# Kernel tuning notes

Measured on AMD Instinct MI355X. Metric: run time of the kernel, lower is better.

Reference implementation:

```python
import jax, jax.numpy as jnp
import numpy as np

EPS = 1e-5
H = 8  # num_heads

def ln(x, g, b):
    m = x.mean(-1, keepdims=True)
    v = ((x - m) ** 2).mean(-1, keepdims=True)
    return (x - m) / jnp.sqrt(v + EPS) * g + b

def gca(qf, kf, p):
    # Gated cross-modal attention (eval mode, dropout off, mask all-True => no mask)
    (nqg, nqb, nkg, nkb, wq, bq, wk, bk, wv, bv, wo, bo,
     wgp, bgp, g1w, g1b, glng, glnb, g2w, g2b) = p
    B, Sq, _ = qf.shape
    Sk = kf.shape[1]
    E = wq.shape[1]
    D = E // H
    qn = ln(qf, nqg, nqb)
    kn = ln(kf, nkg, nkb)
    q = (qn @ wq + bq).reshape(B, Sq, H, D)
    k = (kn @ wk + bk).reshape(B, Sk, H, D)
    v = (kn @ wv + bv).reshape(B, Sk, H, D)
    scores = jnp.einsum('bqhd,bkhd->bhqk', q, k) * (D ** -0.5)
    w = jax.nn.softmax(scores, axis=-1)          # [B,H,Sq,Sk]
    ctx = jnp.einsum('bhqk,bkhd->bqhd', w, v).reshape(B, Sq, E)
    att = ctx @ wo + bo                          # cross-attention output
    qp = qf @ wgp + bgp                          # query projected for gating
    h = jnp.concatenate([qp, att], axis=-1) @ g1w + g1b
    gate = jax.nn.sigmoid(jax.nn.gelu(ln(h, glng, glnb), approximate=False) @ g2w + g2b)
    return qp + gate * att, w

def ff(x, lng, lnb, w1, b1, w2, b2):
    y = jax.nn.gelu(ln(x, lng, lnb) @ w1 + b1, approximate=False)
    return x + (y @ w2 + b2)

def setup_inputs() -> dict:
    B, Sv, St, Vd, Td, F = 8, 1024, 512, 1024, 768, 512
    keys = iter(jax.random.split(jax.random.key(0), 80))
    def nrm(shape):
        return jax.random.normal(next(keys), shape, jnp.float32) * 0.02
    d = {}
    d['vision_features'] = jax.random.normal(next(keys), (B, Sv, Vd), jnp.float32)
    d['text_features'] = jax.random.normal(next(keys), (B, St, Td), jnp.float32)
    def attn_params(pfx, qd, kd, e):
        d[pfx + 'nq_g'] = jnp.ones(qd); d[pfx + 'nq_b'] = jnp.zeros(qd)
        d[pfx + 'nk_g'] = jnp.ones(kd); d[pfx + 'nk_b'] = jnp.zeros(kd)
        d[pfx + 'wq'] = nrm((qd, e)); d[pfx + 'bq'] = jnp.zeros(e)
        d[pfx + 'wk'] = nrm((kd, e)); d[pfx + 'bk'] = jnp.zeros(e)
        d[pfx + 'wv'] = nrm((kd, e)); d[pfx + 'bv'] = jnp.zeros(e)
        d[pfx + 'wo'] = nrm((e, e)); d[pfx + 'bo'] = jnp.zeros(e)
        d[pfx + 'wgp'] = nrm((qd, e)); d[pfx + 'bgp'] = jnp.zeros(e)
        d[pfx + 'g1w'] = nrm((2 * e, e)); d[pfx + 'g1b'] = jnp.zeros(e)
        d[pfx + 'glng'] = jnp.ones(e); d[pfx + 'glnb'] = jnp.zeros(e)
        d[pfx + 'g2w'] = nrm((e, e)); d[pfx + 'g2b'] = jnp.zeros(e)
    attn_params('t2v_', Td, Vd, F)  # text queries attend to vision
    attn_params('v2t_', Vd, Td, F)  # vision queries attend to text
    for pfx in ('vff_', 'tff_'):
        d[pfx + 'lng'] = jnp.ones(F); d[pfx + 'lnb'] = jnp.zeros(F)
        d[pfx + 'w1'] = nrm((F, 4 * F)); d[pfx + 'b1'] = jnp.zeros(4 * F)
        d[pfx + 'w2'] = nrm((4 * F, F)); d[pfx + 'b2'] = jnp.zeros(F)
    return d

def reference(vision_features, text_features,
              t2v_nq_g, t2v_nq_b, t2v_nk_g, t2v_nk_b, t2v_wq, t2v_bq, t2v_wk, t2v_bk, t2v_wv, t2v_bv, t2v_wo, t2v_bo, t2v_wgp, t2v_bgp, t2v_g1w, t2v_g1b, t2v_glng, t2v_glnb, t2v_g2w, t2v_g2b,
              v2t_nq_g, v2t_nq_b, v2t_nk_g, v2t_nk_b, v2t_wq, v2t_bq, v2t_wk, v2t_bk, v2t_wv, v2t_bv, v2t_wo, v2t_bo, v2t_wgp, v2t_bgp, v2t_g1w, v2t_g1b, v2t_glng, v2t_glnb, v2t_g2w, v2t_g2b,
              vff_lng, vff_lnb, vff_w1, vff_b1, vff_w2, vff_b2,
              tff_lng, tff_lnb, tff_w1, tff_b1, tff_w2, tff_b2):
    t2v_p = (t2v_nq_g, t2v_nq_b, t2v_nk_g, t2v_nk_b, t2v_wq, t2v_bq, t2v_wk, t2v_bk, t2v_wv, t2v_bv, t2v_wo, t2v_bo, t2v_wgp, t2v_bgp, t2v_g1w, t2v_g1b, t2v_glng, t2v_glnb, t2v_g2w, t2v_g2b)
    v2t_p = (v2t_nq_g, v2t_nq_b, v2t_nk_g, v2t_nk_b, v2t_wq, v2t_bq, v2t_wk, v2t_bk, v2t_wv, v2t_bv, v2t_wo, v2t_bo, v2t_wgp, v2t_bgp, v2t_g1w, v2t_g1b, v2t_glng, v2t_glnb, v2t_g2w, v2t_g2b)
    text_att, t2v_w = gca(text_features, vision_features, t2v_p)
    vis_att, v2t_w = gca(vision_features, text_features, v2t_p)
    vision_out = ff(vis_att, vff_lng, vff_lnb, vff_w1, vff_b1, vff_w2, vff_b2)
    text_out = ff(text_att, tff_lng, tff_lnb, tff_w1, tff_b1, tff_w2, tff_b2)
    return (vision_out, text_out, t2v_w, v2t_w)
```

## Files before the change

kernel.cpp:

```cpp
#include <hip/hip_runtime.h>
#include <math.h>


typedef __attribute__((ext_vector_type(8))) short s16x8;
typedef __attribute__((ext_vector_type(4))) float f32x4;
typedef __attribute__((ext_vector_type(4))) unsigned short us4;

__device__ __forceinline__ float gelu_exact(float x) {
  return 0.5f * x * (1.0f + erff(x * 0.70710678118654752f));
}
__device__ __forceinline__ float sigmoidf_(float x) {
  return 1.0f / (1.0f + expf(-x));
}
__device__ __forceinline__ unsigned short f2bf(float f) {
  unsigned int u = __float_as_uint(f);
  u += 0x7fffu + ((u >> 16) & 1u);
  return (unsigned short)(u >> 16);
}

template <bool GELU>
__global__ __launch_bounds__(256) void ln_kernel(
    const float* __restrict__ x, const float* __restrict__ g,
    const float* __restrict__ b, unsigned short* __restrict__ out, int cols) {
  const int row = blockIdx.x;
  const float2* xr = (const float2*)(x + (size_t)row * cols);
  const float2* g2 = (const float2*)g;
  const float2* b2 = (const float2*)b;
  const int n2 = cols >> 1;
  const int tid = threadIdx.x;
  float s = 0.f, ss = 0.f;
  for (int c = tid; c < n2; c += 256) {
    float2 v = xr[c];
    s += v.x + v.y;
    ss += v.x * v.x + v.y * v.y;
  }
#pragma unroll
  for (int off = 32; off; off >>= 1) {
    s += __shfl_down(s, off, 64);
    ss += __shfl_down(ss, off, 64);
  }
  __shared__ float rs[4], rss[4], stat[2];
  const int lane = tid & 63, wid = tid >> 6;
  if (lane == 0) {
    rs[wid] = s;
    rss[wid] = ss;
  }
  __syncthreads();
  if (tid == 0) {
    float ts = rs[0] + rs[1] + rs[2] + rs[3];
    float tss = rss[0] + rss[1] + rss[2] + rss[3];
    float m = ts / (float)cols;
    float var = tss / (float)cols - m * m;
    stat[0] = m;
    stat[1] = 1.0f / sqrtf(var + 1e-5f);
  }
  __syncthreads();
  const float m = stat[0], inv = stat[1];
  ushort2* o2 = (ushort2*)(out + (size_t)row * cols);
  for (int c = tid; c < n2; c += 256) {
    float2 v = xr[c];
    float2 gg = g2[c], bb = b2[c];
    float o0 = (v.x - m) * inv * gg.x + bb.x;
    float o1 = (v.y - m) * inv * gg.y + bb.y;
    if (GELU) {
      o0 = gelu_exact(o0);
      o1 = gelu_exact(o1);
    }
    ushort2 r;
    r.x = f2bf(o0);
    r.y = f2bf(o1);
    o2[c] = r;
  }
}

__global__ __launch_bounds__(256) void cast_kernel(
    const float* __restrict__ x, unsigned short* __restrict__ o, int n4) {
  const int stride = gridDim.x * 256;
  for (int i = blockIdx.x * 256 + threadIdx.x; i < n4; i += stride) {
    float4 v = ((const float4*)x)[i];
    us4 r = {f2bf(v.x), f2bf(v.y), f2bf(v.z), f2bf(v.w)};
    ((us4*)o)[i] = r;
  }
}

struct TP {
  const float* s[8];
  unsigned short* d[8];
};
__global__ __launch_bounds__(256) void tc_kernel(TP tp, int R, int C) {
  __shared__ unsigned short tile[32][33];
  const float* src = tp.s[blockIdx.z];
  unsigned short* dst = tp.d[blockIdx.z];
  const int r0 = blockIdx.y * 32, c0 = blockIdx.x * 32;
  const int t = threadIdx.x;
  const int tr = t >> 3, tc4 = (t & 7) * 4;
  float4 v = *(const float4*)(src + (size_t)(r0 + tr) * C + c0 + tc4);
  tile[tr][tc4 + 0] = f2bf(v.x);
  tile[tr][tc4 + 1] = f2bf(v.y);
  tile[tr][tc4 + 2] = f2bf(v.z);
  tile[tr][tc4 + 3] = f2bf(v.w);
  __syncthreads();
  us4 o = {tile[tc4 + 0][tr], tile[tc4 + 1][tr], tile[tc4 + 2][tr],
           tile[tc4 + 3][tr]};
  *(us4*)(dst + (size_t)(c0 + tr) * R + r0 + tc4) = o;
}

template <int SK>
__global__ __launch_bounds__(256) void attn_sm(
    const unsigned short* __restrict__ qp, const unsigned short* __restrict__ kp,
    float* __restrict__ w, unsigned short* __restrict__ wb, int Sq,
    float scale) {
  constexpr int TPW = SK / 64;
  const int z = blockIdx.y, b = z >> 3, h = z & 7;
  const int q0 = blockIdx.x * 16;
  const int t = threadIdx.x, wv = t >> 6, lane = t & 63;
  const int hh = lane >> 4, r16 = lane & 15;
  const unsigned short* qrow =
      qp + (size_t)(b * Sq + q0 + r16) * 512 + h * 64 + 4 * hh;
  s16x8 aq[2];
#pragma unroll
  for (int kt = 0; kt < 2; ++kt) {
    ((unsigned long long*)&aq[kt])[0] =
        *(const unsigned long long*)(qrow + kt * 32);
    ((unsigned long long*)&aq[kt])[1] =
        *(const unsigned long long*)(qrow + kt * 32 + 16);
  }
  const unsigned short* kbase = kp + (size_t)b * SK * 512 + h * 64 + 4 * hh;
  f32x4 sc[TPW];
#pragma unroll
  for (int tl = 0; tl < TPW; ++tl) {
    const unsigned short* krow =
        kbase + (size_t)(wv * (TPW * 16) + tl * 16 + r16) * 512;
    s16x8 b0, b1;
    ((unsigned long long*)&b0)[0] = *(const unsigned long long*)(krow);
    ((unsigned long long*)&b0)[1] = *(const unsigned long long*)(krow + 16);
    ((unsigned long long*)&b1)[0] = *(const unsigned long long*)(krow + 32);
    ((unsigned long long*)&b1)[1] = *(const unsigned long long*)(krow + 48);
    f32x4 a = {};
    a = __builtin_amdgcn_mfma_f32_16x16x32_bf16(aq[0], b0, a, 0, 0, 0);
    a = __builtin_amdgcn_mfma_f32_16x16x32_bf16(aq[1], b1, a, 0, 0, 0);
    sc[tl] = a * scale;
  }
  __shared__ float redM[4][16], redS[4][16];
  float mx[4], sm[4];
#pragma unroll
  for (int q = 0; q < 4; ++q) {
    float m = sc[0][q];
#pragma unroll
    for (int tl = 1; tl < TPW; ++tl) m = fmaxf(m, sc[tl][q]);
    mx[q] = m;
  }
#pragma unroll
  for (int off = 1; off < 16; off <<= 1)
#pragma unroll
    for (int q = 0; q < 4; ++q)
      mx[q] = fmaxf(mx[q], __shfl_xor(mx[q], off, 64));
// ... 35 lines not shown
  float* wrow = w + ((size_t)z * Sq + q0) * SK;
  unsigned short* wbrow = wb + ((size_t)z * Sq + q0) * SK;
#pragma unroll
  for (int tl = 0; tl < TPW; ++tl) {
    const int col = wv * (TPW * 16) + tl * 16 + r16;
#pragma unroll
    for (int q = 0; q < 4; ++q) {
      const float v = sc[tl][q] * inv[q];
      const size_t o = (size_t)(hh * 4 + q) * SK + col;
      wrow[o] = v;
      wbrow[o] = f2bf(v);
    }
  }
}

enum { EPI_B = 0, EPI_BG = 1, EPI_BR = 2, EPI_BGATE = 3, EPI_SC = 4, EPI_KV = 5 };

template <int EPI, int OM, bool CONCAT>
__global__ __launch_bounds__(256) void mm(
    const unsigned short* __restrict__ A0,
    const unsigned short* __restrict__ A1, int lda0, int lda1, int K0, int K,
    const unsigned short* __restrict__ Bt, int ldb,
    const float* __restrict__ bias, const float* __restrict__ bias2,
    const float* __restrict__ X1, const float* __restrict__ X2,
    float* __restrict__ outF, unsigned short* __restrict__ outB,
    unsigned short* __restrict__ outT, int ldc, int skShift, float scale,
    size_t aZb, size_t aZh, size_t bZb, size_t bZh, size_t cZb, size_t cZh) {
  __shared__ unsigned short As[2][64][40];
  __shared__ unsigned short Bs[2][64][40];
  const int z = blockIdx.z;
  const size_t zb = z >> 3, zh = z & 7;
  const int m0 = blockIdx.y * 64, n0 = blockIdx.x * 64;
  const int t = threadIdx.x;
  const int w = t >> 6, lane = t & 63;
  const int h = lane >> 4, r16 = lane & 15;
  const int wm = w >> 1, wn = w & 1;
  const int sr = t >> 2, jr = t & 3;
  const int B0 = (jr < 2) ? (jr * 32) : ((jr - 2) * 32 + 8);
  const unsigned short* Ab =
      A0 + zb * aZb + zh * aZh + (size_t)(m0 + sr) * lda0 + jr * 8;
  const unsigned short* A1b =
      CONCAT ? (A1 + (size_t)(m0 + sr) * lda1 + jr * 8) : nullptr;
  const unsigned short* Bb =
      Bt + zb * bZb + zh * bZh + (size_t)(n0 + sr) * ldb + jr * 8;
  const int NT = K >> 5;
  auto ldA = [&](int tt) -> uint4 {
    const int k0 = tt * 32;
    if (CONCAT && k0 >= K0) return *(const uint4*)(A1b + (k0 - K0));
    return *(const uint4*)(Ab + k0);
  };
  uint4 ua = ldA(0);
  uint4 ub = *(const uint4*)(Bb);
  f32x4 acc[2][2] = {};
  int cur = 0;
  for (int tt = 0; tt < NT; ++tt) {
    {
      char* da = (char*)&As[cur][sr][0] + B0;
      *(unsigned long long*)da = ((const unsigned long long*)&ua)[0];
      *(unsigned long long*)(da + 16) = ((const unsigned long long*)&ua)[1];
      char* db = (char*)&Bs[cur][sr][0] + B0;
      *(unsigned long long*)db = ((const unsigned long long*)&ub)[0];
      *(unsigned long long*)(db + 16) = ((const unsigned long long*)&ub)[1];
    }
    if (tt + 1 < NT) {
      ua = ldA(tt + 1);
      ub = *(const uint4*)(Bb + (tt + 1) * 32);
    }
    __syncthreads();
    s16x8 av[2], bv[2];
#pragma unroll
    for (int i = 0; i < 2; ++i)
      av[i] = *(const s16x8*)&As[cur][wm * 32 + i * 16 + r16][h * 8];
#pragma unroll
    for (int j = 0; j < 2; ++j)
      bv[j] = *(const s16x8*)&Bs[cur][wn * 32 + j * 16 + r16][h * 8];
#pragma unroll
    for (int i = 0; i < 2; ++i)
#pragma unroll
      for (int j = 0; j < 2; ++j)
        acc[i][j] = __builtin_amdgcn_mfma_f32_16x16x32_bf16(av[i], bv[j],
                                                            acc[i][j], 0, 0, 0);
    cur ^= 1;
  }
  const size_t cz = zb * cZb + zh * cZh;
#pragma unroll
  for (int i = 0; i < 2; ++i) {
    const int rr = m0 + wm * 32 + i * 16 + h * 4;
#pragma unroll
    for (int j = 0; j < 2; ++j) {
      const int cc = n0 + wn * 32 + j * 16 + r16;
      if (EPI == EPI_KV) {
        const bool isK = (cc < 512);
        const float bb = isK ? bias[cc] : bias2[cc - 512];
#pragma unroll
        for (int q = 0; q < 4; ++q) {
          const float v = acc[i][j][q] + bb;
          const int r = rr + q;
          if (isK) {
            outB[(size_t)r * 512 + cc] = f2bf(v);
          } else {
            const int b_ = r >> skShift;
            const int sk = r - (b_ << skShift);
            outT[(((size_t)b_ * 512 + (cc - 512)) << skShift) + sk] = f2bf(v);
          }
        }
      } else {
        const float bb = (EPI == EPI_SC) ? 0.f : bias[cc];
#pragma unroll
        for (int q = 0; q < 4; ++q) {
          float v = acc[i][j][q];
          v = (EPI == EPI_SC) ? v * scale : v + bb;
          if (EPI == EPI_BG) v = gelu_exact(v);
          const size_t idx = cz + (size_t)(rr + q) * ldc + cc;
          if (EPI == EPI_BR) v = X1[idx] + v;
          if (EPI == EPI_BGATE) v = X1[idx] + sigmoidf_(v) * X2[idx];
          if (OM & 1) outF[idx] = v;
          if (OM & 2) outB[idx] = f2bf(v);
        }
      }
    }
  }
}

extern "C" void kernel_launch(void* const* d_in, const int* in_sizes, int n_in,
                              void* d_out, int out_size, void* d_ws,
                              size_t ws_size, hipStream_t stream) {
  (void)in_sizes;
  (void)n_in;
  (void)out_size;
  (void)ws_size;
  const int B = 8, Sv = 1024, St = 512, Vd = 1024, Td = 768, E = 512;
  auto inf = [&](int i) { return (const float*)d_in[i]; };
  float* out = (float*)d_out;
  char* ws = (char*)d_ws;
  float* out_vis = out;
  float* out_txt = out + 4194304;
  float* w_t2v = out + 6291456;
  float* w_v2t = out + 39845888;

  const size_t W0 = 0;
  const size_t R1o = 67108864;
  const size_t R2o = 83886080;
  const size_t R3o = 100663296;
  const size_t R4o = 109051904;
  const size_t R5o = 117440512;
  const size_t R6o = 125829120;
  auto U = [&](size_t o) { return (unsigned short*)(ws + o); };
  auto F = [&](size_t o) { return (float*)(ws + o); };

  {
    const int pb = 2;
    const int Sq = St, Sk = Sv, Mq = B * Sq, Mk = B * Sk;
    unsigned short* wq_t = U(R3o + 0);
    unsigned short* wk_t = U(R3o + 786432);
    unsigned short* wv_t = U(R3o + 1835008);
    unsigned short* wo_t = U(R3o + 2883584);
    unsigned short* wgp_t = U(R3o + 3407872);
    unsigned short* g1w_t = U(R3o + 4194304);
    unsigned short* g2w_t = U(R3o + 5242880);
    {
      TP tp{};
      tp.s[0] = inf(pb + 4); tp.d[0] = wq_t;
      tp.s[1] = inf(pb + 12); tp.d[1] = wgp_t;
      tc_kernel<<<dim3(16, 24, 2), 256, 0, stream>>>(tp, 768, 512);
    }
    {
      TP tp{};
      tp.s[0] = inf(pb + 6); tp.d[0] = wk_t;
      tp.s[1] = inf(pb + 8); tp.d[1] = wv_t;
      tp.s[2] = inf(pb + 14); tp.d[2] = g1w_t;
      tc_kernel<<<dim3(16, 32, 3), 256, 0, stream>>>(tp, 1024, 512);
    }
    {
      TP tp{};
      tp.s[0] = inf(pb + 10); tp.d[0] = wo_t;
      tp.s[1] = inf(pb + 18); tp.d[1] = g2w_t;
      tc_kernel<<<dim3(16, 16, 2), 256, 0, stream>>>(tp, 512, 512);
    }
    unsigned short* qn = U(W0);
    unsigned short* kn = U(R1o);
    unsigned short* q_bf = U(R5o);
    unsigned short* k_bf = U(R6o);
    unsigned short* vt = U(R4o);
    unsigned short* w_bf = U(W0);
    unsigned short* ctx_bf = U(R1o);
    float* att_f = F(R2o);
    unsigned short* att_bf = U(W0 + 50331648);
    unsigned short* txt_bf = U(W0);
    float* qp_f = F(R1o + 8388608);
    unsigned short* qp_bf = U(W0 + 58720256);
    float* h_f = F(W0 + 16777216);
    unsigned short* hg = U(W0);

    ln_kernel<false><<<Mq, 256, 0, stream>>>(inf(1), inf(pb + 0), inf(pb + 1),
                                             qn, Td);
    ln_kernel<false><<<Mk, 256, 0, stream>>>(inf(0), inf(pb + 2), inf(pb + 3),
                                             kn, Vd);
    mm<EPI_B, 2, false><<<dim3(8, 64), 256, 0, stream>>>(
        qn, nullptr, Td, 0, Td, Td, wq_t, Td, inf(pb + 5), nullptr, nullptr,
        nullptr, nullptr, q_bf, nullptr, E, 0, 1.f, 0, 0, 0, 0, 0, 0);
    mm<EPI_KV, 0, false><<<dim3(16, 128), 256, 0, stream>>>(
        kn, nullptr, Vd, 0, Vd, Vd, wk_t, Vd, inf(pb + 7), inf(pb + 9),
        nullptr, nullptr, nullptr, k_bf, vt, 0, 10, 1.f, 0, 0, 0, 0, 0, 0);
    attn_sm<1024><<<dim3(Sq / 16, 64), 256, 0, stream>>>(q_bf, k_bf, w_t2v,
                                                         w_bf, Sq, 0.125f);
    mm<EPI_SC, 2, false><<<dim3(1, Sq / 64, 64), 256, 0, stream>>>(
        w_bf, nullptr, Sk, 0, Sk, Sk, vt, Sk, nullptr, nullptr, nullptr,
        nullptr, nullptr, ctx_bf, nullptr, E, 0, 1.f, (size_t)8 * Sq * Sk,
        (size_t)Sq * Sk, (size_t)E * Sk, (size_t)64 * Sk, (size_t)Sq * E, 64);
    mm<EPI_B, 3, false><<<dim3(8, 64), 256, 0, stream>>>(
        ctx_bf, nullptr, E, 0, E, E, wo_t, E, inf(pb + 11), nullptr, nullptr,
        nullptr, att_f, att_bf, nullptr, E, 0, 1.f, 0, 0, 0, 0, 0, 0);
    cast_kernel<<<1024, 256, 0, stream>>>(inf(1), txt_bf, Mq * Td / 4);
    mm<EPI_B, 3, false><<<dim3(8, 64), 256, 0, stream>>>(
        txt_bf, nullptr, Td, 0, Td, Td, wgp_t, Td, inf(pb + 13), nullptr,
        nullptr, nullptr, qp_f, qp_bf, nullptr, E, 0, 1.f, 0, 0, 0, 0, 0, 0);
    mm<EPI_B, 1, true><<<dim3(8, 64), 256, 0, stream>>>(
        qp_bf, att_bf, E, E, E, 2 * E, g1w_t, 2 * E, inf(pb + 15), nullptr,
        nullptr, nullptr, h_f, nullptr, nullptr, E, 0, 1.f, 0, 0, 0, 0, 0, 0);
    ln_kernel<true><<<Mq, 256, 0, stream>>>(h_f, inf(pb + 16), inf(pb + 17),
                                            hg, E);
    mm<EPI_BGATE, 1, false><<<dim3(8, 64), 256, 0, stream>>>(
        hg, nullptr, E, 0, E, E, g2w_t, E, inf(pb + 19), nullptr, qp_f, att_f,
        out_txt, nullptr, nullptr, E, 0, 1.f, 0, 0, 0, 0, 0, 0);
  }
  {
    const int pb = 22;
    const int Sq = Sv, Sk = St, Mq = B * Sv, Mk = B * St;
    unsigned short* wq_t = U(R3o + 0);
    unsigned short* wk_t = U(R3o + 1048576);
    unsigned short* wv_t = U(R3o + 1835008);
    unsigned short* wo_t = U(R3o + 2621440);
    unsigned short* wgp_t = U(R3o + 3145728);
    unsigned short* g1w_t = U(R3o + 4194304);
    unsigned short* g2w_t = U(R3o + 5242880);
    {
      TP tp{};
      tp.s[0] = inf(pb + 4); tp.d[0] = wq_t;
      tp.s[1] = inf(pb + 12); tp.d[1] = wgp_t;
      tp.s[2] = inf(pb + 14); tp.d[2] = g1w_t;
      tc_kernel<<<dim3(16, 32, 3), 256, 0, stream>>>(tp, 1024, 512);
    }
    {
      TP tp{};
      tp.s[0] = inf(pb + 6); tp.d[0] = wk_t;
      tp.s[1] = inf(pb + 8); tp.d[1] = wv_t;
      tc_kernel<<<dim3(16, 24, 2), 256, 0, stream>>>(tp, 768, 512);
    }
    {
      TP tp{};
      tp.s[0] = inf(pb + 10); tp.d[0] = wo_t;
      tp.s[1] = inf(pb + 18); tp.d[1] = g2w_t;
      tc_kernel<<<dim3(16, 16, 2), 256, 0, stream>>>(tp, 512, 512);
    }
    unsigned short* qn = U(W0);
    unsigned short* kn = U(R1o);
    unsigned short* q_bf = U(R5o);
    unsigned short* k_bf = U(R6o);
    unsigned short* vt = U(R4o);
    unsigned short* w_bf = U(W0);
    unsigned short* ctx_bf = U(R1o);
    float* att_f = F(R2o);
    unsigned short* att_bf = U(W0 + 50331648);
    unsigned short* vis_bf = U(W0);
    float* qp_f = F(R1o);
    unsigned short* qp_bf = U(W0 + 58720256);
    float* h_f = F(W0 + 16777216);
    unsigned short* hg = U(W0);

    ln_kernel<false><<<Mq, 256, 0, stream>>>(inf(0), inf(pb + 0), inf(pb + 1),
                                             qn, Vd);
    ln_kernel<false><<<Mk, 256, 0, stream>>>(inf(1), inf(pb + 2), inf(pb + 3),
                                             kn, Td);
    mm<EPI_B, 2, false><<<dim3(8, 128), 256, 0, stream>>>(
        qn, nullptr, Vd, 0, Vd, Vd, wq_t, Vd, inf(pb + 5), nullptr, nullptr,
        nullptr, nullptr, q_bf, nullptr, E, 0, 1.f, 0, 0, 0, 0, 0, 0);
    mm<EPI_KV, 0, false><<<dim3(16, 64), 256, 0, stream>>>(
        kn, nullptr, Td, 0, Td, Td, wk_t, Td, inf(pb + 7), inf(pb + 9),
        nullptr, nullptr, nullptr, k_bf, vt, 0, 9, 1.f, 0, 0, 0, 0, 0, 0);
    attn_sm<512><<<dim3(Sq / 16, 64), 256, 0, stream>>>(q_bf, k_bf, w_v2t,
                                                        w_bf, Sq, 0.125f);
    mm<EPI_SC, 2, false><<<dim3(1, Sq / 64, 64), 256, 0, stream>>>(
        w_bf, nullptr, Sk, 0, Sk, Sk, vt, Sk, nullptr, nullptr, nullptr,
        nullptr, nullptr, ctx_bf, nullptr, E, 0, 1.f, (size_t)8 * Sq * Sk,
        (size_t)Sq * Sk, (size_t)E * Sk, (size_t)64 * Sk, (size_t)Sq * E, 64);
    mm<EPI_B, 3, false><<<dim3(8, 128), 256, 0, stream>>>(
        ctx_bf, nullptr, E, 0, E, E, wo_t, E, inf(pb + 11), nullptr, nullptr,
        nullptr, att_f, att_bf, nullptr, E, 0, 1.f, 0, 0, 0, 0, 0, 0);
    cast_kernel<<<2048, 256, 0, stream>>>(inf(0), vis_bf, Mq * Vd / 4);
    mm<EPI_B, 3, false><<<dim3(8, 128), 256, 0, stream>>>(
        vis_bf, nullptr, Vd, 0, Vd, Vd, wgp_t, Vd, inf(pb + 13), nullptr,
        nullptr, nullptr, qp_f, qp_bf, nullptr, E, 0, 1.f, 0, 0, 0, 0, 0, 0);
    mm<EPI_B, 1, true><<<dim3(8, 128), 256, 0, stream>>>(
        qp_bf, att_bf, E, E, E, 2 * E, g1w_t, 2 * E, inf(pb + 15), nullptr,
        nullptr, nullptr, h_f, nullptr, nullptr, E, 0, 1.f, 0, 0, 0, 0, 0, 0);
    ln_kernel<true><<<Mq, 256, 0, stream>>>(h_f, inf(pb + 16), inf(pb + 17),
                                            hg, E);
    mm<EPI_BGATE, 1, false><<<dim3(8, 128), 256, 0, stream>>>(
        hg, nullptr, E, 0, E, E, g2w_t, E, inf(pb + 19), nullptr, qp_f, att_f,
        out_vis, nullptr, nullptr, E, 0, 1.f, 0, 0, 0, 0, 0, 0);
  }
  {
    unsigned short* vw1_t = U(R3o + 0);
    unsigned short* vw2_t = U(R3o + 2097152);
    unsigned short* tw1_t = U(R3o + 4194304);
    unsigned short* tw2_t = U(R3o + 6291456);
    {
      TP tp{};
      tp.s[0] = inf(44); tp.d[0] = vw1_t;
      tp.s[1] = inf(50); tp.d[1] = tw1_t;
      tc_kernel<<<dim3(64, 16, 2), 256, 0, stream>>>(tp, 512, 2048);
    }
    {
      TP tp{};
      tp.s[0] = inf(46); tp.d[0] = vw2_t;
      tp.s[1] = inf(52); tp.d[1] = tw2_t;
      tc_kernel<<<dim3(16, 64, 2), 256, 0, stream>>>(tp, 2048, 512);
    }
    unsigned short* lnv = U(W0);
    unsigned short* y_v = U(W0 + 8388608);
    unsigned short* lnt = U(W0 + 41943040);
    unsigned short* y_t = U(W0 + 46137344);
    ln_kernel<false><<<8192, 256, 0, stream>>>(out_vis, inf(42), inf(43), lnv,
                                               512);
    mm<EPI_BG, 2, false><<<dim3(32, 128), 256, 0, stream>>>(
        lnv, nullptr, 512, 0, 512, 512, vw1_t, 512, inf(45), nullptr, nullptr,
        nullptr, nullptr, y_v, nullptr, 2048, 0, 1.f, 0, 0, 0, 0, 0, 0);
    mm<EPI_BR, 1, false><<<dim3(8, 128), 256, 0, stream>>>(
        y_v, nullptr, 2048, 0, 2048, 2048, vw2_t, 2048, inf(47), nullptr,
        out_vis, nullptr, out_vis, nullptr, nullptr, 512, 0, 1.f, 0, 0, 0, 0,
        0, 0);
    ln_kernel<false><<<4096, 256, 0, stream>>>(out_txt, inf(48), inf(49), lnt,
                                               512);
    mm<EPI_BG, 2, false><<<dim3(32, 64), 256, 0, stream>>>(
        lnt, nullptr, 512, 0, 512, 512, tw1_t, 512, inf(51), nullptr, nullptr,
        nullptr, nullptr, y_t, nullptr, 2048, 0, 1.f, 0, 0, 0, 0, 0, 0);
    mm<EPI_BR, 1, false><<<dim3(8, 64), 256, 0, stream>>>(
        y_t, nullptr, 2048, 0, 2048, 2048, tw2_t, 2048, inf(53), nullptr,
        out_txt, nullptr, out_txt, nullptr, nullptr, 512, 0, 1.f, 0, 0, 0, 0,
        0, 0);
  }
}
```

Measured before the change: 1.108 ms.

## Batch both attention directions into shared multi-job kernel launches

Both cross-attention branches and both FFNs now run inside the same kernels. Matmuls, layernorms, casts, attention softmax and the weight transposes each take job descriptors and pick a job per block, which cuts the launch count and fills the GPU better for the small grids. Workspace buffers are laid out separately for each direction so the two directions can run at once. This costs more workspace memory, and some blocks in the merged grids exit early or do a per-block job lookup.

```diff
diff --git a/kernel.cpp b/kernel.cpp
--- a/kernel.cpp
+++ b/kernel.cpp
@@ -18,14 +18,23 @@
   return (unsigned short)(u >> 16);
 }
 
+struct LNJ {
+  const float* x[4];
+  const float* g[4];
+  const float* b[4];
+  unsigned short* o[4];
+  int cols[4];
+  int pfx[5];
+};
 template <bool GELU>
-__global__ __launch_bounds__(256) void ln_kernel(
-    const float* __restrict__ x, const float* __restrict__ g,
-    const float* __restrict__ b, unsigned short* __restrict__ out, int cols) {
-  const int row = blockIdx.x;
-  const float2* xr = (const float2*)(x + (size_t)row * cols);
-  const float2* g2 = (const float2*)g;
-  const float2* b2 = (const float2*)b;
+__global__ __launch_bounds__(256) void ln_multi(LNJ p) {
+  int row = blockIdx.x, ji = 0;
+  while (row >= p.pfx[ji + 1]) ++ji;
+  const int lrow = row - p.pfx[ji];
+  const int cols = p.cols[ji];
+  const float2* xr = (const float2*)(p.x[ji] + (size_t)lrow * cols);
+  const float2* g2 = (const float2*)p.g[ji];
+  const float2* b2 = (const float2*)p.b[ji];
   const int n2 = cols >> 1;
   const int tid = threadIdx.x;
   float s = 0.f, ss = 0.f;
@@ -56,7 +65,7 @@
   }
   __syncthreads();
   const float m = stat[0], inv = stat[1];
-  ushort2* o2 = (ushort2*)(out + (size_t)row * cols);
+  ushort2* o2 = (ushort2*)(p.o[ji] + (size_t)lrow * cols);
   for (int c = tid; c < n2; c += 256) {
     float2 v = xr[c];
     float2 gg = g2[c], bb = b2[c];
@@ -73,8 +82,16 @@
   }
 }
 
-__global__ __launch_bounds__(256) void cast_kernel(
-    const float* __restrict__ x, unsigned short* __restrict__ o, int n4) {
+struct CJ {
+  const float* s[2];
+  unsigned short* d[2];
+  int n4[2];
+};
+__global__ __launch_bounds__(256) void cast2(CJ p) {
+  const int z = blockIdx.z;
+  const float* x = p.s[z];
+  unsigned short* o = p.d[z];
+  const int n4 = p.n4[z];
   const int stride = gridDim.x * 256;
   for (int i = blockIdx.x * 256 + threadIdx.x; i < n4; i += stride) {
     float4 v = ((const float4*)x)[i];
@@ -83,17 +100,25 @@
   }
 }
 
-struct TP {
-  const float* s[8];
-  unsigned short* d[8];
+struct TCJ {
+  const float* s[18];
+  unsigned int doff[18];
+  unsigned short cy[18], cx[18];
+  unsigned short pfx[19];
 };
-__global__ __launch_bounds__(256) void tc_kernel(TP tp, int R, int C) {
+__global__ __launch_bounds__(256) void tc_all(TCJ p, unsigned short* wt) {
   __shared__ unsigned short tile[32][33];
-  const float* src = tp.s[blockIdx.z];
-  unsigned short* dst = tp.d[blockIdx.z];
-  const int r0 = blockIdx.y * 32, c0 = blockIdx.x * 32;
-  const int t = threadIdx.x;
-  const int tr = t >> 3, tc4 = (t & 7) * 4;
+  int t = blockIdx.x, ji = 0;
+  while (t >= p.pfx[ji + 1]) ++ji;
+  const int lt = t - p.pfx[ji];
+  const int cx = p.cx[ji];
+  const int ty = lt / cx, tx = lt - ty * cx;
+  const int R = p.cy[ji] * 32, C = cx * 32;
+  const float* src = p.s[ji];
+  unsigned short* dst = (unsigned short*)((char*)wt + p.doff[ji]);
+  const int r0 = ty * 32, c0 = tx * 32;
+  const int tid = threadIdx.x;
+  const int tr = tid >> 3, tc4 = (tid & 7) * 4;
   float4 v = *(const float4*)(src + (size_t)(r0 + tr) * C + c0 + tc4);
   tile[tr][tc4 + 0] = f2bf(v.x);
   tile[tr][tc4 + 1] = f2bf(v.y);
@@ -106,13 +131,13 @@
 }
 
 template <int SK>
-__global__ __launch_bounds__(256) void attn_sm(
+__device__ __forceinline__ void attn_body(
     const unsigned short* __restrict__ qp, const unsigned short* __restrict__ kp,
-    float* __restrict__ w, unsigned short* __restrict__ wb, int Sq,
-    float scale) {
+    float* __restrict__ w, unsigned short* __restrict__ wb, int Sq, int z,
+    int qblk) {
   constexpr int TPW = SK / 64;
-  const int z = blockIdx.y, b = z >> 3, h = z & 7;
-  const int q0 = blockIdx.x * 16;
+  const int b = z >> 3, h = z & 7;
+  const int q0 = qblk * 16;
   const int t = threadIdx.x, wv = t >> 6, lane = t & 63;
   const int hh = lane >> 4, r16 = lane & 15;
   const unsigned short* qrow =
@@ -139,7 +164,7 @@
     f32x4 a = {};
     a = __builtin_amdgcn_mfma_f32_16x16x32_bf16(aq[0], b0, a, 0, 0, 0);
     a = __builtin_amdgcn_mfma_f32_16x16x32_bf16(aq[1], b1, a, 0, 0, 0);
-    sc[tl] = a * scale;
+    sc[tl] = a * 0.125f;
   }
   __shared__ float redM[4][16], redS[4][16];
   float mx[4], sm[4];
@@ -205,23 +230,48 @@
   }
 }
 
+__global__ __launch_bounds__(256) void attn2(
+    const unsigned short* q0, const unsigned short* k0, float* w0,
+    unsigned short* wb0, const unsigned short* q1, const unsigned short* k1,
+    float* w1, unsigned short* wb1) {
+  const int y = blockIdx.y;
+  if (y < 64) {
+    if (blockIdx.x >= 32) return;
+    attn_body<1024>(q0, k0, w0, wb0, 512, y, blockIdx.x);
+  } else {
+    attn_body<512>(q1, k1, w1, wb1, 1024, y - 64, blockIdx.x);
+  }
+}
+
 enum { EPI_B = 0, EPI_BG = 1, EPI_BR = 2, EPI_BGATE = 3, EPI_SC = 4, EPI_KV = 5 };
 
-template <int EPI, int OM, bool CONCAT>
-__global__ __launch_bounds__(256) void mm(
-    const unsigned short* __restrict__ A0,
-    const unsigned short* __restrict__ A1, int lda0, int lda1, int K0, int K,
-    const unsigned short* __restrict__ Bt, int ldb,
-    const float* __restrict__ bias, const float* __restrict__ bias2,
-    const float* __restrict__ X1, const float* __restrict__ X2,
-    float* __restrict__ outF, unsigned short* __restrict__ outB,
-    unsigned short* __restrict__ outT, int ldc, int skShift, float scale,
-    size_t aZb, size_t aZh, size_t bZb, size_t bZh, size_t cZb, size_t cZh) {
+struct MMJ {
+  const unsigned short *A0, *A1, *Bt;
+  const float *bias, *bias2, *X1, *X2;
+  float* outF;
+  unsigned short *outB, *outT;
+  int lda0, lda1, K0, K, ldb, ldc, skShift, ny, nz;
+  float scale;
+  size_t aZb, aZh, bZb, bZh, cZb, cZh;
+};
+
+template <int EPI, int OM, bool CONCAT, bool ZSPLIT>
+__global__ __launch_bounds__(256) void mm2(MMJ j0, MMJ j1) {
+  int y = blockIdx.y, z = blockIdx.z;
+  bool side;
+  if (ZSPLIT) {
+    side = (z >= j0.nz);
+    if (side) z -= j0.nz;
+    if (y >= (side ? j1.ny : j0.ny)) return;
+  } else {
+    side = (y >= j0.ny);
+    if (side) y -= j0.ny;
+  }
+  const MMJ& j = side ? j1 : j0;
   __shared__ unsigned short As[2][64][40];
   __shared__ unsigned short Bs[2][64][40];
-  const int z = blockIdx.z;
   const size_t zb = z >> 3, zh = z & 7;
-  const int m0 = blockIdx.y * 64, n0 = blockIdx.x * 64;
+  const int m0 = y * 64, n0 = blockIdx.x * 64;
   const int t = threadIdx.x;
   const int w = t >> 6, lane = t & 63;
   const int h = lane >> 4, r16 = lane & 15;
@@ -229,15 +279,15 @@
   const int sr = t >> 2, jr = t & 3;
   const int B0 = (jr < 2) ? (jr * 32) : ((jr - 2) * 32 + 8);
   const unsigned short* Ab =
-      A0 + zb * aZb + zh * aZh + (size_t)(m0 + sr) * lda0 + jr * 8;
+      j.A0 + zb * j.aZb + zh * j.aZh + (size_t)(m0 + sr) * j.lda0 + jr * 8;
   const unsigned short* A1b =
-      CONCAT ? (A1 + (size_t)(m0 + sr) * lda1 + jr * 8) : nullptr;
+      CONCAT ? (j.A1 + (size_t)(m0 + sr) * j.lda1 + jr * 8) : nullptr;
   const unsigned short* Bb =
-      Bt + zb * bZb + zh * bZh + (size_t)(n0 + sr) * ldb + jr * 8;
-  const int NT = K >> 5;
+      j.Bt + zb * j.bZb + zh * j.bZh + (size_t)(n0 + sr) * j.ldb + jr * 8;
+  const int NT = j.K >> 5;
   auto ldA = [&](int tt) -> uint4 {
     const int k0 = tt * 32;
-    if (CONCAT && k0 >= K0) return *(const uint4*)(A1b + (k0 - K0));
+    if (CONCAT && k0 >= j.K0) return *(const uint4*)(A1b + (k0 - j.K0));
     return *(const uint4*)(Ab + k0);
   };
   uint4 ua = ldA(0);
@@ -263,50 +313,51 @@
     for (int i = 0; i < 2; ++i)
       av[i] = *(const s16x8*)&As[cur][wm * 32 + i * 16 + r16][h * 8];
 #pragma unroll
-    for (int j = 0; j < 2; ++j)
-      bv[j] = *(const s16x8*)&Bs[cur][wn * 32 + j * 16 + r16][h * 8];
+    for (int jx = 0; jx < 2; ++jx)
+      bv[jx] = *(const s16x8*)&Bs[cur][wn * 32 + jx * 16 + r16][h * 8];
 #pragma unroll
     for (int i = 0; i < 2; ++i)
 #pragma unroll
-      for (int j = 0; j < 2; ++j)
-        acc[i][j] = __builtin_amdgcn_mfma_f32_16x16x32_bf16(av[i], bv[j],
-                                                            acc[i][j], 0, 0, 0);
+      for (int jx = 0; jx < 2; ++jx)
+        acc[i][jx] = __builtin_amdgcn_mfma_f32_16x16x32_bf16(av[i], bv[jx],
+                                                             acc[i][jx], 0, 0, 0);
     cur ^= 1;
   }
-  const size_t cz = zb * cZb + zh * cZh;
+  const size_t cz = zb * j.cZb + zh * j.cZh;
 #pragma unroll
   for (int i = 0; i < 2; ++i) {
     const int rr = m0 + wm * 32 + i * 16 + h * 4;
 #pragma unroll
-    for (int j = 0; j < 2; ++j) {
-      const int cc = n0 + wn * 32 + j * 16 + r16;
+    for (int jx = 0; jx < 2; ++jx) {
+      const int cc = n0 + wn * 32 + jx * 16 + r16;
       if (EPI == EPI_KV) {
         const bool isK = (cc < 512);
-        const float bb = isK ? bias[cc] : bias2[cc - 512];
+        const float bb = isK ? j.bias[cc] : j.bias2[cc - 512];
 #pragma unroll
         for (int q = 0; q < 4; ++q) {
-          const float v = acc[i][j][q] + bb;
+          const float v = acc[i][jx][q] + bb;
           const int r = rr + q;
           if (isK) {
-            outB[(size_t)r * 512 + cc] = f2bf(v);
+            j.outB[(size_t)r * 512 + cc] = f2bf(v);
           } else {
-            const int b_ = r >> skShift;
-            const int sk = r - (b_ << skShift);
-            outT[(((size_t)b_ * 512 + (cc - 512)) << skShift) + sk] = f2bf(v);
+            const int b_ = r >> j.skShift;
+            const int sk = r - (b_ << j.skShift);
+            j.outT[(((size_t)b_ * 512 + (cc - 512)) << j.skShift) + sk] =
+                f2bf(v);
           }
         }
       } else {
-        const float bb = (EPI == EPI_SC) ? 0.f : bias[cc];
+        const float bb = (EPI == EPI_SC) ? 0.f : j.bias[cc];
 #pragma unroll
         for (int q = 0; q < 4; ++q) {
-          float v = acc[i][j][q];
-          v = (EPI == EPI_SC) ? v * scale : v + bb;
+          float v = acc[i][jx][q];
+          v = (EPI == EPI_SC) ? v * j.scale : v + bb;
           if (EPI == EPI_BG) v = gelu_exact(v);
-          const size_t idx = cz + (size_t)(rr + q) * ldc + cc;
-          if (EPI == EPI_BR) v = X1[idx] + v;
-          if (EPI == EPI_BGATE) v = X1[idx] + sigmoidf_(v) * X2[idx];
-          if (OM & 1) outF[idx] = v;
-          if (OM & 2) outB[idx] = f2bf(v);
+          const size_t idx = cz + (size_t)(rr + q) * j.ldc + cc;
+          if (EPI == EPI_BR) v = j.X1[idx] + v;
+          if (EPI == EPI_BGATE) v = j.X1[idx] + sigmoidf_(v) * j.X2[idx];
+          if (OM & 1) j.outF[idx] = v;
+          if (OM & 2) j.outB[idx] = f2bf(v);
         }
       }
     }
@@ -320,7 +371,6 @@
   (void)n_in;
   (void)out_size;
   (void)ws_size;
-  const int B = 8, Sv = 1024, St = 512, Vd = 1024, Td = 768, E = 512;
   auto inf = [&](int i) { return (const float*)d_in[i]; };
   float* out = (float*)d_out;
   char* ws = (char*)d_ws;
@@ -329,206 +379,200 @@
   float* w_t2v = out + 6291456;
   float* w_v2t = out + 39845888;
 
-  const size_t W0 = 0;
-  const size_t R1o = 67108864;
-  const size_t R2o = 83886080;
-  const size_t R3o = 100663296;
-  const size_t R4o = 109051904;
-  const size_t R5o = 117440512;
-  const size_t R6o = 125829120;
-  auto U = [&](size_t o) { return (unsigned short*)(ws + o); };
-  auto F = [&](size_t o) { return (float*)(ws + o); };
-
-  {
-    const int pb = 2;
-    const int Sq = St, Sk = Sv, Mq = B * Sq, Mk = B * Sk;
-    unsigned short* wq_t = U(R3o + 0);
-    unsigned short* wk_t = U(R3o + 786432);
-    unsigned short* wv_t = U(R3o + 1835008);
-    unsigned short* wo_t = U(R3o + 2883584);
-    unsigned short* wgp_t = U(R3o + 3407872);
-    unsigned short* g1w_t = U(R3o + 4194304);
-    unsigned short* g2w_t = U(R3o + 5242880);
-    {
-      TP tp{};
-      tp.s[0] = inf(pb + 4); tp.d[0] = wq_t;
-      tp.s[1] = inf(pb + 12); tp.d[1] = wgp_t;
-      tc_kernel<<<dim3(16, 24, 2), 256, 0, stream>>>(tp, 768, 512);
-    }
-    {
-      TP tp{};
-      tp.s[0] = inf(pb + 6); tp.d[0] = wk_t;
-      tp.s[1] = inf(pb + 8); tp.d[1] = wv_t;
-      tp.s[2] = inf(pb + 14); tp.d[2] = g1w_t;
-      tc_kernel<<<dim3(16, 32, 3), 256, 0, stream>>>(tp, 1024, 512);
-    }
-    {
-      TP tp{};
-      tp.s[0] = inf(pb + 10); tp.d[0] = wo_t;
-      tp.s[1] = inf(pb + 18); tp.d[1] = g2w_t;
-      tc_kernel<<<dim3(16, 16, 2), 256, 0, stream>>>(tp, 512, 512);
-    }
-    unsigned short* qn = U(W0);
-    unsigned short* kn = U(R1o);
-    unsigned short* q_bf = U(R5o);
-    unsigned short* k_bf = U(R6o);
-    unsigned short* vt = U(R4o);
-    unsigned short* w_bf = U(W0);
-    unsigned short* ctx_bf = U(R1o);
-    float* att_f = F(R2o);
-    unsigned short* att_bf = U(W0 + 50331648);
-    unsigned short* txt_bf = U(W0);
-    float* qp_f = F(R1o + 8388608);
-    unsigned short* qp_bf = U(W0 + 58720256);
-    float* h_f = F(W0 + 16777216);
-    unsigned short* hg = U(W0);
-
-    ln_kernel<false><<<Mq, 256, 0, stream>>>(inf(1), inf(pb + 0), inf(pb + 1),
-                                             qn, Td);
-    ln_kernel<false><<<Mk, 256, 0, stream>>>(inf(0), inf(pb + 2), inf(pb + 3),
-                                             kn, Vd);
-    mm<EPI_B, 2, false><<<dim3(8, 64), 256, 0, stream>>>(
-        qn, nullptr, Td, 0, Td, Td, wq_t, Td, inf(pb + 5), nullptr, nullptr,
-        nullptr, nullptr, q_bf, nullptr, E, 0, 1.f, 0, 0, 0, 0, 0, 0);
-    mm<EPI_KV, 0, false><<<dim3(16, 128), 256, 0, stream>>>(
-        kn, nullptr, Vd, 0, Vd, Vd, wk_t, Vd, inf(pb + 7), inf(pb + 9),
-        nullptr, nullptr, nullptr, k_bf, vt, 0, 10, 1.f, 0, 0, 0, 0, 0, 0);
-    attn_sm<1024><<<dim3(Sq / 16, 64), 256, 0, stream>>>(q_bf, k_bf, w_t2v,
-                                                         w_bf, Sq, 0.125f);
-    mm<EPI_SC, 2, false><<<dim3(1, Sq / 64, 64), 256, 0, stream>>>(
-        w_bf, nullptr, Sk, 0, Sk, Sk, vt, Sk, nullptr, nullptr, nullptr,
-        nullptr, nullptr, ctx_bf, nullptr, E, 0, 1.f, (size_t)8 * Sq * Sk,
-        (size_t)Sq * Sk, (size_t)E * Sk, (size_t)64 * Sk, (size_t)Sq * E, 64);
-    mm<EPI_B, 3, false><<<dim3(8, 64), 256, 0, stream>>>(
-        ctx_bf, nullptr, E, 0, E, E, wo_t, E, inf(pb + 11), nullptr, nullptr,
-        nullptr, att_f, att_bf, nullptr, E, 0, 1.f, 0, 0, 0, 0, 0, 0);
-    cast_kernel<<<1024, 256, 0, stream>>>(inf(1), txt_bf, Mq * Td / 4);
-    mm<EPI_B, 3, false><<<dim3(8, 64), 256, 0, stream>>>(
-        txt_bf, nullptr, Td, 0, Td, Td, wgp_t, Td, inf(pb + 13), nullptr,
-        nullptr, nullptr, qp_f, qp_bf, nullptr, E, 0, 1.f, 0, 0, 0, 0, 0, 0);
-    mm<EPI_B, 1, true><<<dim3(8, 64), 256, 0, stream>>>(
-        qp_bf, att_bf, E, E, E, 2 * E, g1w_t, 2 * E, inf(pb + 15), nullptr,
-        nullptr, nullptr, h_f, nullptr, nullptr, E, 0, 1.f, 0, 0, 0, 0, 0, 0);
-    ln_kernel<true><<<Mq, 256, 0, stream>>>(h_f, inf(pb + 16), inf(pb + 17),
-                                            hg, E);
-    mm<EPI_BGATE, 1, false><<<dim3(8, 64), 256, 0, stream>>>(
-        hg, nullptr, E, 0, E, E, g2w_t, E, inf(pb + 19), nullptr, qp_f, att_f,
-        out_txt, nullptr, nullptr, E, 0, 1.f, 0, 0, 0, 0, 0, 0);
-  }
-  {
-    const int pb = 22;
-    const int Sq = Sv, Sk = St, Mq = B * Sv, Mk = B * St;
-    unsigned short* wq_t = U(R3o + 0);
-    unsigned short* wk_t = U(R3o + 1048576);
-    unsigned short* wv_t = U(R3o + 1835008);
-    unsigned short* wo_t = U(R3o + 2621440);
-    unsigned short* wgp_t = U(R3o + 3145728);
-    unsigned short* g1w_t = U(R3o + 4194304);
-    unsigned short* g2w_t = U(R3o + 5242880);
-    {
-      TP tp{};
-      tp.s[0] = inf(pb + 4); tp.d[0] = wq_t;
-      tp.s[1] = inf(pb + 12); tp.d[1] = wgp_t;
-      tp.s[2] = inf(pb + 14); tp.d[2] = g1w_t;
-      tc_kernel<<<dim3(16, 32, 3), 256, 0, stream>>>(tp, 1024, 512);
-    }
-    {
-      TP tp{};
-      tp.s[0] = inf(pb + 6); tp.d[0] = wk_t;
-      tp.s[1] = inf(pb + 8); tp.d[1] = wv_t;
-      tc_kernel<<<dim3(16, 24, 2), 256, 0, stream>>>(tp, 768, 512);
-    }
-    {
-      TP tp{};
-      tp.s[0] = inf(pb + 10); tp.d[0] = wo_t;
-      tp.s[1] = inf(pb + 18); tp.d[1] = g2w_t;
-      tc_kernel<<<dim3(16, 16, 2), 256, 0, stream>>>(tp, 512, 512);
-    }
-    unsigned short* qn = U(W0);
-    unsigned short* kn = U(R1o);
-    unsigned short* q_bf = U(R5o);
-    unsigned short* k_bf = U(R6o);
-    unsigned short* vt = U(R4o);
-    unsigned short* w_bf = U(W0);
-    unsigned short* ctx_bf = U(R1o);
-    float* att_f = F(R2o);
-    unsigned short* att_bf = U(W0 + 50331648);
-    unsigned short* vis_bf = U(W0);
-    float* qp_f = F(R1o);
-    unsigned short* qp_bf = U(W0 + 58720256);
-    float* h_f = F(W0 + 16777216);
-    unsigned short* hg = U(W0);
-
-    ln_kernel<false><<<Mq, 256, 0, stream>>>(inf(0), inf(pb + 0), inf(pb + 1),
-                                             qn, Vd);
-    ln_kernel<false><<<Mk, 256, 0, stream>>>(inf(1), inf(pb + 2), inf(pb + 3),
-                                             kn, Td);
-    mm<EPI_B, 2, false><<<dim3(8, 128), 256, 0, stream>>>(
-        qn, nullptr, Vd, 0, Vd, Vd, wq_t, Vd, inf(pb + 5), nullptr, nullptr,
-        nullptr, nullptr, q_bf, nullptr, E, 0, 1.f, 0, 0, 0, 0, 0, 0);
-    mm<EPI_KV, 0, false><<<dim3(16, 64), 256, 0, stream>>>(
-        kn, nullptr, Td, 0, Td, Td, wk_t, Td, inf(pb + 7), inf(pb + 9),
-        nullptr, nullptr, nullptr, k_bf, vt, 0, 9, 1.f, 0, 0, 0, 0, 0, 0);
-    attn_sm<512><<<dim3(Sq / 16, 64), 256, 0, stream>>>(q_bf, k_bf, w_v2t,
-                                                        w_bf, Sq, 0.125f);
-    mm<EPI_SC, 2, false><<<dim3(1, Sq / 64, 64), 256, 0, stream>>>(
-        w_bf, nullptr, Sk, 0, Sk, Sk, vt, Sk, nullptr, nullptr, nullptr,
-        nullptr, nullptr, ctx_bf, nullptr, E, 0, 1.f, (size_t)8 * Sq * Sk,
-        (size_t)Sq * Sk, (size_t)E * Sk, (size_t)64 * Sk, (size_t)Sq * E, 64);
-    mm<EPI_B, 3, false><<<dim3(8, 128), 256, 0, stream>>>(
-        ctx_bf, nullptr, E, 0, E, E, wo_t, E, inf(pb + 11), nullptr, nullptr,
-        nullptr, att_f, att_bf, nullptr, E, 0, 1.f, 0, 0, 0, 0, 0, 0);
-    cast_kernel<<<2048, 256, 0, stream>>>(inf(0), vis_bf, Mq * Vd / 4);
-    mm<EPI_B, 3, false><<<dim3(8, 128), 256, 0, stream>>>(
-        vis_bf, nullptr, Vd, 0, Vd, Vd, wgp_t, Vd, inf(pb + 13), nullptr,
-        nullptr, nullptr, qp_f, qp_bf, nullptr, E, 0, 1.f, 0, 0, 0, 0, 0, 0);
-    mm<EPI_B, 1, true><<<dim3(8, 128), 256, 0, stream>>>(
-        qp_bf, att_bf, E, E, E, 2 * E, g1w_t, 2 * E, inf(pb + 15), nullptr,
-        nullptr, nullptr, h_f, nullptr, nullptr, E, 0, 1.f, 0, 0, 0, 0, 0, 0);
-    ln_kernel<true><<<Mq, 256, 0, stream>>>(h_f, inf(pb + 16), inf(pb + 17),
-                                            hg, E);
-    mm<EPI_BGATE, 1, false><<<dim3(8, 128), 256, 0, stream>>>(
-        hg, nullptr, E, 0, E, E, g2w_t, E, inf(pb + 19), nullptr, qp_f, att_f,
-        out_vis, nullptr, nullptr, E, 0, 1.f, 0, 0, 0, 0, 0, 0);
-  }
-  {
-    unsigned short* vw1_t = U(R3o + 0);
-    unsigned short* vw2_t = U(R3o + 2097152);
-    unsigned short* tw1_t = U(R3o + 4194304);
-    unsigned short* tw2_t = U(R3o + 6291456);
-    {
-      TP tp{};
-      tp.s[0] = inf(44); tp.d[0] = vw1_t;
-      tp.s[1] = inf(50); tp.d[1] = tw1_t;
-      tc_kernel<<<dim3(64, 16, 2), 256, 0, stream>>>(tp, 512, 2048);
-    }
-    {
-      TP tp{};
-      tp.s[0] = inf(46); tp.d[0] = vw2_t;
-      tp.s[1] = inf(52); tp.d[1] = tw2_t;
-      tc_kernel<<<dim3(16, 64, 2), 256, 0, stream>>>(tp, 2048, 512);
-    }
-    unsigned short* lnv = U(W0);
-    unsigned short* y_v = U(W0 + 8388608);
-    unsigned short* lnt = U(W0 + 41943040);
-    unsigned short* y_t = U(W0 + 46137344);
-    ln_kernel<false><<<8192, 256, 0, stream>>>(out_vis, inf(42), inf(43), lnv,
-                                               512);
-    mm<EPI_BG, 2, false><<<dim3(32, 128), 256, 0, stream>>>(
-        lnv, nullptr, 512, 0, 512, 512, vw1_t, 512, inf(45), nullptr, nullptr,
-        nullptr, nullptr, y_v, nullptr, 2048, 0, 1.f, 0, 0, 0, 0, 0, 0);
-    mm<EPI_BR, 1, false><<<dim3(8, 128), 256, 0, stream>>>(
-        y_v, nullptr, 2048, 0, 2048, 2048, vw2_t, 2048, inf(47), nullptr,
-        out_vis, nullptr, out_vis, nullptr, nullptr, 512, 0, 1.f, 0, 0, 0, 0,
-        0, 0);
-    ln_kernel<false><<<4096, 256, 0, stream>>>(out_txt, inf(48), inf(49), lnt,
-                                               512);
-    mm<EPI_BG, 2, false><<<dim3(32, 64), 256, 0, stream>>>(
-        lnt, nullptr, 512, 0, 512, 512, tw1_t, 512, inf(51), nullptr, nullptr,
-        nullptr, nullptr, y_t, nullptr, 2048, 0, 1.f, 0, 0, 0, 0, 0, 0);
-    mm<EPI_BR, 1, false><<<dim3(8, 64), 256, 0, stream>>>(
-        y_t, nullptr, 2048, 0, 2048, 2048, tw2_t, 2048, inf(53), nullptr,
-        out_txt, nullptr, out_txt, nullptr, nullptr, 512, 0, 1.f, 0, 0, 0, 0,
-        0, 0);
-  }
-}
+  const size_t MBy = 1048576;
+  auto U = [&](size_t mb) { return (unsigned short*)(ws + mb * MBy); };
+  auto F = [&](size_t mb) { return (float*)(ws + mb * MBy); };
+  unsigned short* wt = U(0);
+  const size_t T2V = 0, V2T = 6291456, FFW = 12582912;
+  unsigned short* qn0 = U(20);
+  unsigned short* kn0 = U(26);
+  unsigned short* qn1 = U(42);
+  unsigned short* kn1 = U(58);
+  unsigned short* txt_bf = U(64);
+  unsigned short* vis_bf = U(70);
+  unsigned short* q_bf0 = U(86);
+  unsigned short* q_bf1 = U(90);
+  unsigned short* k_bf0 = U(98);
+  unsigned short* k_bf1 = U(106);
+  unsigned short* vt0 = U(110);
+  unsigned short* vt1 = U(118);
+  unsigned short* w_bf0 = U(122);
+  unsigned short* w_bf1 = U(186);
+  unsigned short* ctx0 = U(250);
+  unsigned short* ctx1 = U(254);
+  float* att_f0 = F(262);
+  unsigned short* att_bf0 = U(270);
+  float* att_f1 = F(274);
+  unsigned short* att_bf1 = U(290);
+  float* qp_f0 = F(298);
+  unsigned short* qp_bf0 = U(306);
+  float* qp_f1 = F(310);
+  unsigned short* qp_bf1 = U(326);
+  float* h_f0 = F(334);
+  float* h_f1 = F(342);
+  unsigned short* hg0 = U(358);
+  unsigned short* hg1 = U(362);
+  unsigned short* lnv = U(370);
+  unsigned short* lnt = U(378);
+  unsigned short* y_v = U(382);
+  unsigned short* y_t = U(414);
+
+  auto mkj = []() { MMJ j{}; j.scale = 1.f; j.nz = 1; return j; };
+
+  {
+    TCJ p{};
+    const int srcIdx[18] = {6, 8, 10, 12, 14, 16, 20, 26, 28, 30, 32, 34,
+                            36, 40, 44, 46, 50, 52};
+    const unsigned int doff[18] = {
+        T2V + 0, T2V + 786432, T2V + 1835008, T2V + 2883584, T2V + 3407872,
+        T2V + 4194304, T2V + 5242880, V2T + 0, V2T + 1048576, V2T + 1835008,
+        V2T + 2621440, V2T + 3145728, V2T + 4194304, V2T + 5242880,
+        FFW + 0, FFW + 2097152, FFW + 4194304, FFW + 6291456};
+    const unsigned short cy[18] = {24, 32, 32, 16, 24, 32, 16, 32, 24, 24,
+                                   16, 32, 32, 16, 16, 64, 16, 64};
+    const unsigned short cx[18] = {16, 16, 16, 16, 16, 16, 16, 16, 16, 16,
+                                   16, 16, 16, 16, 64, 16, 64, 16};
+    unsigned short acc = 0;
+    for (int i = 0; i < 18; ++i) {
+      p.s[i] = inf(srcIdx[i]);
+      p.doff[i] = doff[i];
+      p.cy[i] = cy[i];
+      p.cx[i] = cx[i];
+      p.pfx[i] = acc;
+      acc += cy[i] * cx[i];
+    }
+    p.pfx[18] = acc;
+    tc_all<<<acc, 256, 0, stream>>>(p, wt);
+  }
+  {
+    LNJ p{};
+    p.x[0] = inf(1); p.g[0] = inf(2); p.b[0] = inf(3); p.o[0] = qn0; p.cols[0] = 768;
+    p.x[1] = inf(0); p.g[1] = inf(4); p.b[1] = inf(5); p.o[1] = kn0; p.cols[1] = 1024;
+    p.x[2] = inf(0); p.g[2] = inf(22); p.b[2] = inf(23); p.o[2] = qn1; p.cols[2] = 1024;
+    p.x[3] = inf(1); p.g[3] = inf(24); p.b[3] = inf(25); p.o[3] = kn1; p.cols[3] = 768;
+    p.pfx[0] = 0; p.pfx[1] = 4096; p.pfx[2] = 12288; p.pfx[3] = 20480; p.pfx[4] = 24576;
+    ln_multi<false><<<24576, 256, 0, stream>>>(p);
+  }
+  {
+    CJ p{};
+    p.s[0] = inf(1); p.d[0] = txt_bf; p.n4[0] = 4096 * 768 / 4;
+    p.s[1] = inf(0); p.d[1] = vis_bf; p.n4[1] = 8192 * 1024 / 4;
+    cast2<<<dim3(2048, 1, 2), 256, 0, stream>>>(p);
+  }
+  {
+    MMJ a = mkj(), b = mkj();
+    a.A0 = qn0; a.lda0 = 768; a.K = 768; a.Bt = wt + T2V / 2; a.ldb = 768;
+    a.bias = inf(7); a.outB = q_bf0; a.ldc = 512; a.ny = 64;
+    b.A0 = qn1; b.lda0 = 1024; b.K = 1024; b.Bt = wt + V2T / 2; b.ldb = 1024;
+    b.bias = inf(27); b.outB = q_bf1; b.ldc = 512; b.ny = 128;
+    mm2<EPI_B, 2, false, false><<<dim3(8, 192), 256, 0, stream>>>(a, b);
+  }
+  {
+    MMJ a = mkj(), b = mkj();
+    a.A0 = kn0; a.lda0 = 1024; a.K = 1024;
+    a.Bt = wt + (T2V + 786432) / 2; a.ldb = 1024;
+    a.bias = inf(9); a.bias2 = inf(11); a.outB = k_bf0; a.outT = vt0;
+    a.skShift = 10; a.ny = 128;
+    b.A0 = kn1; b.lda0 = 768; b.K = 768;
+    b.Bt = wt + (V2T + 1048576) / 2; b.ldb = 768;
+    b.bias = inf(29); b.bias2 = inf(31); b.outB = k_bf1; b.outT = vt1;
+    b.skShift = 9; b.ny = 64;
+    mm2<EPI_KV, 0, false, false><<<dim3(16, 192), 256, 0, stream>>>(a, b);
+  }
+  attn2<<<dim3(64, 128), 256, 0, stream>>>(q_bf0, k_bf0, w_t2v, w_bf0, q_bf1,
+                                           k_bf1, w_v2t, w_bf1);
+  {
+    MMJ a = mkj(), b = mkj();
+    a.A0 = w_bf0; a.lda0 = 1024; a.K = 1024; a.Bt = vt0; a.ldb = 1024;
+    a.outB = ctx0; a.ldc = 512; a.ny = 8; a.nz = 64;
+    a.aZb = (size_t)8 * 512 * 1024; a.aZh = 512 * 1024;
+    a.bZb = 512 * 1024; a.bZh = 64 * 1024;
+    a.cZb = 512 * 512; a.cZh = 64;
+    b.A0 = w_bf1; b.lda0 = 512; b.K = 512; b.Bt = vt1; b.ldb = 512;
+    b.outB = ctx1; b.ldc = 512; b.ny = 16; b.nz = 64;
+    b.aZb = (size_t)8 * 1024 * 512; b.aZh = 1024 * 512;
+    b.bZb = 512 * 512; b.bZh = 64 * 512;
+    b.cZb = 1024 * 512; b.cZh = 64;
+    mm2<EPI_SC, 2, false, true><<<dim3(1, 16, 128), 256, 0, stream>>>(a, b);
+  }
+  {
+    MMJ a = mkj(), b = mkj();
+    a.A0 = ctx0; a.lda0 = 512; a.K = 512;
+    a.Bt = wt + (T2V + 2883584) / 2; a.ldb = 512;
+    a.bias = inf(13); a.outF = att_f0; a.outB = att_bf0; a.ldc = 512; a.ny = 64;
+    b.A0 = ctx1; b.lda0 = 512; b.K = 512;
+    b.Bt = wt + (V2T + 2621440) / 2; b.ldb = 512;
+    b.bias = inf(33); b.outF = att_f1; b.outB = att_bf1; b.ldc = 512;
+    b.ny = 128;
+    mm2<EPI_B, 3, false, false><<<dim3(8, 192), 256, 0, stream>>>(a, b);
+  }
+  {
+    MMJ a = mkj(), b = mkj();
+    a.A0 = txt_bf; a.lda0 = 768; a.K = 768;
+    a.Bt = wt + (T2V + 3407872) / 2; a.ldb = 768;
+    a.bias = inf(15); a.outF = qp_f0; a.outB = qp_bf0; a.ldc = 512; a.ny = 64;
+    b.A0 = vis_bf; b.lda0 = 1024; b.K = 1024;
+    b.Bt = wt + (V2T + 3145728) / 2; b.ldb = 1024;
+    b.bias = inf(35); b.outF = qp_f1; b.outB = qp_bf1; b.ldc = 512; b.ny = 128;
+    mm2<EPI_B, 3, false, false><<<dim3(8, 192), 256, 0, stream>>>(a, b);
+  }
+  {
+    MMJ a = mkj(), b = mkj();
+    a.A0 = qp_bf0; a.A1 = att_bf0; a.lda0 = 512; a.lda1 = 512; a.K0 = 512;
+    a.K = 1024; a.Bt = wt + (T2V + 4194304) / 2; a.ldb = 1024;
+    a.bias = inf(17); a.outF = h_f0; a.ldc = 512; a.ny = 64;
+    b.A0 = qp_bf1; b.A1 = att_bf1; b.lda0 = 512; b.lda1 = 512; b.K0 = 512;
+    b.K = 1024; b.Bt = wt + (V2T + 4194304) / 2; b.ldb = 1024;
+    b.bias = inf(37); b.outF = h_f1; b.ldc = 512; b.ny = 128;
+    mm2<EPI_B, 1, true, false><<<dim3(8, 192), 256, 0, stream>>>(a, b);
+  }
+  {
+    LNJ p{};
+    p.x[0] = h_f0; p.g[0] = inf(18); p.b[0] = inf(19); p.o[0] = hg0; p.cols[0] = 512;
+    p.x[1] = h_f1; p.g[1] = inf(38); p.b[1] = inf(39); p.o[1] = hg1; p.cols[1] = 512;
+    p.x[2] = h_f0; p.g[2] = inf(18); p.b[2] = inf(19); p.o[2] = hg0; p.cols[2] = 512;
+    p.x[3] = p.x[2]; p.g[3] = p.g[2]; p.b[3] = p.b[2]; p.o[3] = p.o[2]; p.cols[3] = 512;
+    p.pfx[0] = 0; p.pfx[1] = 4096; p.pfx[2] = 12288; p.pfx[3] = 12288; p.pfx[4] = 12288;
+    ln_multi<true><<<12288, 256, 0, stream>>>(p);
+  }
+  {
+    MMJ a = mkj(), b = mkj();
+    a.A0 = hg0; a.lda0 = 512; a.K = 512;
+    a.Bt = wt + (T2V + 5242880) / 2; a.ldb = 512;
+    a.bias = inf(21); a.X1 = qp_f0; a.X2 = att_f0; a.outF = out_txt;
+    a.ldc = 512; a.ny = 64;
+    b.A0 = hg1; b.lda0 = 512; b.K = 512;
+    b.Bt = wt + (V2T + 5242880) / 2; b.ldb = 512;
+    b.bias = inf(41); b.X1 = qp_f1; b.X2 = att_f1; b.outF = out_vis;
+    b.ldc = 512; b.ny = 128;
+    mm2<EPI_BGATE, 1, false, false><<<dim3(8, 192), 256, 0, stream>>>(a, b);
+  }
+  {
+    LNJ p{};
+    p.x[0] = out_vis; p.g[0] = inf(42); p.b[0] = inf(43); p.o[0] = lnv; p.cols[0] = 512;
+    p.x[1] = out_txt; p.g[1] = inf(48); p.b[1] = inf(49); p.o[1] = lnt; p.cols[1] = 512;
+    p.x[2] = out_vis; p.g[2] = inf(42); p.b[2] = inf(43); p.o[2] = lnv; p.cols[2] = 512;
+    p.x[3] = p.x[2]; p.g[3] = p.g[2]; p.b[3] = p.b[2]; p.o[3] = p.o[2]; p.cols[3] = 512;
+    p.pfx[0] = 0; p.pfx[1] = 8192; p.pfx[2] = 12288; p.pfx[3] = 12288; p.pfx[4] = 12288;
+    ln_multi<false><<<12288, 256, 0, stream>>>(p);
+  }
+  {
+    MMJ a = mkj(), b = mkj();
+    a.A0 = lnv; a.lda0 = 512; a.K = 512; a.Bt = wt + FFW / 2; a.ldb = 512;
+    a.bias = inf(45); a.outB = y_v; a.ldc = 2048; a.ny = 128;
+    b.A0 = lnt; b.lda0 = 512; b.K = 512;
+    b.Bt = wt + (FFW + 4194304) / 2; b.ldb = 512;
+    b.bias = inf(51); b.outB = y_t; b.ldc = 2048; b.ny = 64;
+    mm2<EPI_BG, 2, false, false><<<dim3(32, 192), 256, 0, stream>>>(a, b);
+  }
+  {
+    MMJ a = mkj(), b = mkj();
+    a.A0 = y_v; a.lda0 = 2048; a.K = 2048;
+    a.Bt = wt + (FFW + 2097152) / 2; a.ldb = 2048;
+    a.bias = inf(47); a.X1 = out_vis; a.outF = out_vis; a.ldc = 512; a.ny = 128;
+    b.A0 = y_t; b.lda0 = 2048; b.K = 2048;
+    b.Bt = wt + (FFW + 6291456) / 2; b.ldb = 2048;
+    b.bias = inf(53); b.X1 = out_txt; b.outF = out_txt; b.ldc = 512; b.ny = 64;
+    mm2<EPI_BR, 1, false, false><<<dim3(8, 192), 256, 0, stream>>>(a, b);
+  }
+}
```

New measurement: 1.097 ms. Within noise of the previous version (-1.1%).
